# Kernel tuning notes

Hardware: AMD Instinct MI355X
Metric: run time of the kernel (lower is better)

The kernel has to match this reference:

```python
import jax, jax.numpy as jnp
import numpy as np

# SFNO (modulus) with spectral_transform='fft', filter_type='non-linear', scale_factor=1,
# hard_thresholding_fraction=1.0 (no mode truncation), instance_norm, inner_skip='linear',
# outer_skip='identity', use_mlp=True, encoder_layers=1, pos_embed, big_skip.
B, CIN, COUT, H, W = 1, 2, 2, 181, 360
E, HID, L = 128, 256, 4   # embed_dim, int(mlp_ratio*embed_dim), num_layers
EPS = 1e-6


def _inorm(x, w, b):
    # InstanceNorm2d(affine=True, eps=1e-6): per-(batch,channel) stats over H,W
    mu = jnp.mean(x, axis=(-2, -1), keepdims=True)
    var = jnp.var(x, axis=(-2, -1), keepdims=True)
    xh = (x - mu) * jax.lax.rsqrt(var + EPS)
    return xh * w[None, :, None, None] + b[None, :, None, None]


def _conv1x1(x, w, b=None):
    y = jnp.einsum('bihw,oi->bohw', x, w)
    return y if b is None else y + b[None, :, None, None]


def _cmul(z, w):
    # complex channel mixing; w stored as [2(re/im), c_in, c_out] float
    return jnp.einsum('bihw,io->bohw', z, w[0] + 1j * w[1])


def _crelu(z):
    # ComplexReLU mode='real': relu on real part, imaginary part passes through
    return jax.lax.complex(jax.nn.relu(z.real), z.imag)


def _block(x, p):
    (n0w, n0b, w0, w1, wout, isw, isb, n1w, n1b, fc1w, fc1b, fc2w, fc2b) = p
    xn = _inorm(x, n0w, n0b)
    # SpectralAttention2d (bias=False): rfft2 -> complex MLP over channels -> irfft2
    z = jnp.fft.rfft2(xn, axes=(-2, -1), norm='ortho')   # [B,E,H,W//2+1] complex
    h = _crelu(_cmul(z, w0))
    h = _crelu(_cmul(h, w1))
    y = jnp.fft.irfft2(_cmul(h, wout), s=(H, W), axes=(-2, -1), norm='ortho')
    y = y + _conv1x1(xn, isw, isb)                        # inner skip (linear 1x1 conv)
    y = _inorm(y, n1w, n1b)
    y = _conv1x1(jax.nn.gelu(_conv1x1(y, fc1w, fc1b), approximate=False), fc2w, fc2b)  # MLP
    return y + xn                                         # outer skip (identity on filter residual)


def _forward(x, enc_w0, enc_b0, enc_w1, pos_embed, n0w, n0b, w0, w1, wout,
             isw, isb, n1w, n1b, fc1w, fc1b, fc2w, fc2b, dec_w0, dec_b0, dec_w1):
    resid = x                                              # big skip
    h = jax.nn.gelu(_conv1x1(x, enc_w0, enc_b0), approximate=False)
    h = _conv1x1(h, enc_w1) + pos_embed                    # encoder (final conv bias=False) + pos embed
    def body(c, p):
        return _block(c, p), None
    h, _ = jax.lax.scan(body, h, (n0w, n0b, w0, w1, wout, isw, isb, n1w, n1b,
                                  fc1w, fc1b, fc2w, fc2b))
    h = jnp.concatenate([h, resid], axis=1)                # big skip concat
    h = jax.nn.gelu(_conv1x1(h, dec_w0, dec_b0), approximate=False)
    return _conv1x1(h, dec_w1)                             # decoder final conv bias=False


def setup_inputs() -> dict:
    key = jax.random.key(0)
    ks = jax.random.split(key, 16)
    s = 0.02  # scale used for spectral weights in SpectralAttention2d
    rn = lambda k, shp, sc: (sc * jax.random.normal(k, shp)).astype(jnp.float32)
    return {
        'x': rn(ks[0], (B, CIN, H, W), 1.0),
        'enc_w0': rn(ks[1], (E, CIN), 0.1),
        'enc_b0': jnp.zeros((E,), jnp.float32),
        'enc_w1': rn(ks[2], (E, E), 0.05),
        'pos_embed': rn(ks[3], (1, E, H, W), s),
        'n0w': jnp.ones((L, E), jnp.float32), 'n0b': jnp.zeros((L, E), jnp.float32),
        'w0': rn(ks[4], (L, 2, E, HID), s),
        'w1': rn(ks[5], (L, 2, HID, HID), s),
        'wout': rn(ks[6], (L, 2, HID, E), s),
        'isw': rn(ks[7], (L, E, E), 0.05), 'isb': jnp.zeros((L, E), jnp.float32),
        'n1w': jnp.ones((L, E), jnp.float32), 'n1b': jnp.zeros((L, E), jnp.float32),
        'fc1w': rn(ks[8], (L, HID, E), 0.05), 'fc1b': jnp.zeros((L, HID), jnp.float32),
        'fc2w': rn(ks[9], (L, E, HID), 0.05), 'fc2b': jnp.zeros((L, E), jnp.float32),
        'dec_w0': rn(ks[10], (E, E + CIN), 0.05),
        'dec_b0': jnp.zeros((E,), jnp.float32),
        'dec_w1': rn(ks[11], (COUT, E), 0.05),
    }


def reference(x, enc_w0, enc_b0, enc_w1, pos_embed, n0w, n0b, w0, w1, wout,
              isw, isb, n1w, n1b, fc1w, fc1b, fc2w, fc2b, dec_w0, dec_b0, dec_w1):
    return _forward(x, enc_w0, enc_b0, enc_w1, pos_embed, n0w, n0b, w0, w1, wout,
                    isw, isb, n1w, n1b, fc1w, fc1b, fc2w, fc2b, dec_w0, dec_b0, dec_w1)
```

## Files before the change

kernel.cpp:

```cpp
#include <hip/hip_runtime.h>
#include <math.h>

#define NP 65160
#define NPAD 65280

typedef unsigned short u16;
typedef __attribute__((ext_vector_type(8))) short bf16x8;
typedef __attribute__((ext_vector_type(8))) unsigned short us8;
typedef __attribute__((ext_vector_type(4))) float f32x4;

__device__ __forceinline__ u16 f2bf(float f){
    unsigned u = __builtin_bit_cast(unsigned, f);
    return (u16)((u + 0x7FFFu + ((u>>16)&1u)) >> 16);
}
__device__ __forceinline__ float bf2f(u16 h){
    unsigned u = ((unsigned)h)<<16;
    return __builtin_bit_cast(float, u);
}
__device__ __forceinline__ float gelu_f(float x){
    return 0.5f*x*(1.0f+erff(x*0.70710678118654752f));
}

__global__ void k_zero(u16* __restrict__ p, long n){
    long i = ((long)blockIdx.x*256 + threadIdx.x)*8;
    if(i+8 <= n){ us8 z = {0,0,0,0,0,0,0,0}; *(us8*)(p+i) = z; }
}

__global__ void k_pack_twf(u16* __restrict__ dst){
    int i = blockIdx.x*256+threadIdx.x; if(i >= 48*384*8) return;
    int e = i&7, n = (i>>3)%384, kg = i/(384*8);
    int k = kg*8+e, kw = n>>1, q = n&1;
    float v = 0.0f;
    if(k < 360 && kw < 181){
        float inv = 1.0f/sqrtf(65160.0f);
        float th = 6.28318530717958647692f*(float)((k*kw)%360)/360.0f;
        v = q ? -sinf(th)*inv : cosf(th)*inv;
    }
    dst[i] = f2bf(v);
}
__global__ void k_pack_thf(u16* __restrict__ dst){
    int i = blockIdx.x*256+threadIdx.x; if(i >= 64*384*8) return;
    int e = i&7, n = (i>>3)%384, kg = i/(384*8);
    int k = kg*8+e;
    float v = 0.0f;
    if(k < 362 && n < 362){
        int h = k>>1, q = k&1, kh = n>>1, p = n&1;
        float th = 6.28318530717958647692f*(float)((h*kh)%181)/181.0f;
        float c = cosf(th), s = sinf(th);
        v = (q==0) ? (p==0? c : -s) : (p==0? s : c);
    }
    dst[i] = f2bf(v);
}
__global__ void k_pack_thi(u16* __restrict__ dst){
    int i = blockIdx.x*256+threadIdx.x; if(i >= 48*384*8) return;
    int e = i&7, n = (i>>3)%384, kg = i/(384*8);
    int k = kg*8+e;
    float v = 0.0f;
    if(k < 362 && n < 362){
        int kh = k>>1, p = k&1, h = n>>1, q = n&1;
        float th = 6.28318530717958647692f*(float)((kh*h)%181)/181.0f;
        float c = cosf(th), s = sinf(th);
        v = (q==0) ? (p==0? c : -s) : (p==0? s : c);
    }
    dst[i] = f2bf(v);
}
__global__ void k_pack_twi(u16* __restrict__ dst){
    int i = blockIdx.x*256+threadIdx.x; if(i >= 48*384*8) return;
    int e = i&7, n = (i>>3)%384, kg = i/(384*8);
    int k = kg*8+e, kw = k>>1, q = k&1;
    float v = 0.0f;
    if(k < 362 && n < 360){
        float inv = 1.0f/sqrtf(65160.0f);
        float eps = (kw==0 || kw==180) ? 1.0f : 2.0f;
        float th = 6.28318530717958647692f*(float)((n*kw)%360)/360.0f;
        v = q ? -eps*sinf(th)*inv : eps*cosf(th)*inv;
    }
    dst[i] = f2bf(v);
}
__global__ void k_pack_cw(const float* __restrict__ src, u16* __restrict__ dst,
                          int CIN, int COUT, int lss, int lsd){
    int z = blockIdx.z;
    int Npad = 2*COUT, KG = (2*CIN)/8;
    int tot = KG*Npad*8;
    int i = blockIdx.x*256+threadIdx.x; if(i >= tot) return;
    int e = i&7, n = (i>>3)%Npad, kg = i/(Npad*8);
    int k = kg*8+e, ci = k>>1, q = k&1, co = n>>1, p = n&1;
    float re = src[(size_t)z*lss + ci*COUT + co];
    float im = src[(size_t)z*lss + CIN*COUT + ci*COUT + co];
    float v = (p==0) ? (q==0? re : -im) : (q==0? im : re);
    dst[(size_t)z*lsd + i] = f2bf(v);
}
__global__ void k_pack_rw(const float* __restrict__ src, u16* __restrict__ dst,
                          int Nn, int Ks, int KG, int lss, int lsd){
    int z = blockIdx.z;
    int tot = KG*Nn*8;
    int i = blockIdx.x*256+threadIdx.x; if(i >= tot) return;
    int e = i&7, n = (i>>3)%Nn, kg = i/(Nn*8);
    int k = kg*8+e;
    float v = (k < Ks) ? src[(size_t)z*lss + n*Ks + k] : 0.0f;
    dst[(size_t)z*lsd + i] = f2bf(v);
}

__global__ void k_enc0(const float* __restrict__ x, const float* __restrict__ w,
                       const float* __restrict__ b, u16* __restrict__ out){
    int i = blockIdx.x*256+threadIdx.x;
    if(i >= NP*16) return;
    int p = i>>4, c8 = (i&15)*8;
    float x0 = x[p], x1 = x[NP+p];
    us8 o;
    #pragma unroll
    for(int j=0;j<8;j++){
        int e = c8+j;
        float v = w[e*2]*x0 + w[e*2+1]*x1 + b[e];
        o[j] = f2bf(gelu_f(v));
    }
    *(us8*)(out + (size_t)p*128 + c8) = o;
}
__global__ void k_xt2(const float* __restrict__ x, u16* __restrict__ dst){
    int p = blockIdx.x*256+threadIdx.x; if(p >= NP) return;
    us8 z = {0,0,0,0,0,0,0,0};
    z[0] = f2bf(x[p]); z[1] = f2bf(x[NP+p]);
    *(us8*)(dst + (size_t)p*32) = z;
    us8 z2 = {0,0,0,0,0,0,0,0};
    *(us8*)(dst + (size_t)p*32 + 8)  = z2;
    *(us8*)(dst + (size_t)p*32 + 16) = z2;
    *(us8*)(dst + (size_t)p*32 + 24) = z2;
}
__global__ void k_dec1(const u16* __restrict__ hid, const float* __restrict__ w,
                       float* __restrict__ out){
    int p = blockIdx.x*256+threadIdx.x; if(p >= NP) return;
    float a0=0.0f, a1=0.0f;
    #pragma unroll 4
    for(int k8=0;k8<16;k8++){
        us8 v = *(const us8*)(hid + (size_t)p*128 + k8*8);
        #pragma unroll
        for(int j=0;j<8;j++){
            float f = bf2f(v[j]);
            a0 = fmaf(w[k8*8+j], f, a0);
            a1 = fmaf(w[128+k8*8+j], f, a1);
        }
    }
    out[p] = a0; out[NP+p] = a1;
}

__global__ __launch_bounds__(256) void k_apply_t(
    const u16* __restrict__ X, u16* __restrict__ outp, u16* __restrict__ outc,
    const float* __restrict__ stat, const float* __restrict__ gw, const float* __restrict__ gb)
{
    __shared__ u16 T[128][72];
    __shared__ float SA_[128], SB_[128];
    int t = threadIdx.x;
    if(t < 128){
        float mu = stat[t]*(1.0f/(float)NP);
        float var = stat[128+t]*(1.0f/(float)NP) - mu*mu;
        var = fmaxf(var, 0.0f);
        float rstd = 1.0f/sqrtf(var + 1e-6f);
        float a = rstd*gw[t];
        SA_[t] = a; SB_[t] = gb[t] - mu*a;
    }
    __syncthreads();
    int p0 = blockIdx.x*64;
    int pl = t>>2, cc = (t&3)*32;
    int p = p0 + pl;
    if(p < NP){
        #pragma unroll
        for(int jj=0;jj<4;jj++){
            us8 v = *(const us8*)(X + (size_t)p*128 + cc + jj*8);
            us8 o;
            #pragma unroll
            for(int j=0;j<8;j++){
                int c = cc + jj*8 + j;
                o[j] = f2bf(fmaf(bf2f(v[j]), SA_[c], SB_[c]));
            }
            *(us8*)(outp + (size_t)p*128 + cc + jj*8) = o;
            #pragma unroll
            for(int j=0;j<8;j++) T[cc+jj*8+j][pl] = o[j];
        }
    }
    __syncthreads();
    int c = t>>1, half = t&1;
    int pbase = p0 + half*32;
    #pragma unroll
    for(int jj=0;jj<4;jj++){
        int pp = pbase + jj*8;
        if(pp + 8 <= NP){
            int hh = pp/360, ww = pp - hh*360;
            *(us8*)(outc + ((size_t)c*192 + hh)*384 + ww) = *(const us8*)(&T[c][half*32 + jj*8]);
        }
    }
}
__global__ __launch_bounds__(256) void k_post(const float* __restrict__ src, u16* __restrict__ dst){
    __shared__ u16 T[128][72];
    int t = threadIdx.x;
    int p0 = blockIdx.x*64;
    int c = t>>1, half = t&1;
    int pbase = p0 + half*32;
    #pragma unroll
    for(int jj=0;jj<4;jj++){
        int pp = pbase + jj*8;
        us8 v = {0,0,0,0,0,0,0,0};
        if(pp + 8 <= NP){
            #pragma unroll
            for(int j=0;j<8;j++) v[j] = f2bf(src[(size_t)c*NP + pp + j]);
        }
        *(us8*)(&T[c][half*32 + jj*8]) = v;
    }
    __syncthreads();
    int pl = t>>2, cc = (t&3)*32;
    int p = p0 + pl;
    if(p < NP){
        #pragma unroll
        for(int jj=0;jj<4;jj++){
            us8 o;
            #pragma unroll
            for(int j=0;j<8;j++) o[j] = T[cc+jj*8+j][pl];
            *(us8*)(dst + (size_t)p*128 + cc + jj*8) = o;
        }
    }
}

__global__ __launch_bounds__(512, 4) void k_smlp(
    const u16* __restrict__ A3, const u16* __restrict__ W0,
    const u16* __restrict__ W1, const u16* __restrict__ WO,
    u16* __restrict__ A4)
{
    __shared__ u16 Hs0[32*520];
    __shared__ u16 Hs1[32*520];
    int tid = threadIdx.x;
    int l = tid & 63, wn = tid >> 6;
    int lm = l & 15, kg = l >> 4;
    int m0 = blockIdx.x * 32;

    f32x4 acc[2][4];
    #pragma unroll
    for(int f=0;f<2;f++)
        #pragma unroll
        for(int j2=0;j2<4;j2++) acc[f][j2] = (f32x4){0.f,0.f,0.f,0.f};
    {
        const u16* ap = A3 + (size_t)(m0 + lm)*256 + kg*8;
        #pragma unroll
        for(int k0=0;k0<256;k0+=32){
            bf16x8 af[2];
            #pragma unroll
            for(int f=0;f<2;f++) af[f] = *(const bf16x8*)(ap + f*16*256 + k0);
            const u16* Bb = W0 + (size_t)((k0>>3)+kg)*4096 + (wn*64+lm)*8;
            #pragma unroll
            for(int j2=0;j2<4;j2++){
                bf16x8 bf = *(const bf16x8*)(Bb + j2*128);
                #pragma unroll
                for(int f=0;f<2;f++)
                    acc[f][j2] = __builtin_amdgcn_mfma_f32_16x16x32_bf16(af[f], bf, acc[f][j2], 0,0,0);
            }
        }
    }
    #pragma unroll
    for(int f=0;f<2;f++)
        #pragma unroll
        for(int j2=0;j2<4;j2++)
            #pragma unroll
            for(int r=0;r<4;r++){
                int row = f*16 + kg*4 + r;
                int col = wn*64 + j2*16 + lm;
                float v = acc[f][j2][r];
                if(!(col&1)) v = fmaxf(v, 0.0f);
                Hs0[row*520 + col] = f2bf(v);
            }
    __syncthreads();
    #pragma unroll
    for(int f=0;f<2;f++)
        #pragma unroll
        for(int j2=0;j2<4;j2++) acc[f][j2] = (f32x4){0.f,0.f,0.f,0.f};
    #pragma unroll 2
    for(int k0=0;k0<512;k0+=32){
        bf16x8 af[2];
        #pragma unroll
        for(int f=0;f<2;f++) af[f] = *(const bf16x8*)(&Hs0[(f*16+lm)*520 + k0 + kg*8]);
        const u16* Bb = W1 + (size_t)((k0>>3)+kg)*4096 + (wn*64+lm)*8;
        #pragma unroll
        for(int j2=0;j2<4;j2++){
            bf16x8 bf = *(const bf16x8*)(Bb + j2*128);
            #pragma unroll
            for(int f=0;f<2;f++)
                acc[f][j2] = __builtin_amdgcn_mfma_f32_16x16x32_bf16(af[f], bf, acc[f][j2], 0,0,0);
        }
    }
    #pragma unroll
    for(int f=0;f<2;f++)
        #pragma unroll
        for(int j2=0;j2<4;j2++)
            #pragma unroll
            for(int r=0;r<4;r++){
                int row = f*16 + kg*4 + r;
                int col = wn*64 + j2*16 + lm;
                float v = acc[f][j2][r];
                if(!(col&1)) v = fmaxf(v, 0.0f);
                Hs1[row*520 + col] = f2bf(v);
            }
    __syncthreads();
    f32x4 acc3[2][2];
    #pragma unroll
    for(int f=0;f<2;f++)
        #pragma unroll
        for(int j2=0;j2<2;j2++) acc3[f][j2] = (f32x4){0.f,0.f,0.f,0.f};
    #pragma unroll 2
    for(int k0=0;k0<512;k0+=32){
        bf16x8 af[2];
        #pragma unroll
        for(int f=0;f<2;f++) af[f] = *(const bf16x8*)(&Hs1[(f*16+lm)*520 + k0 + kg*8]);
        const u16* Bb = WO + (size_t)((k0>>3)+kg)*2048 + (wn*32+lm)*8;
        #pragma unroll
        for(int j2=0;j2<2;j2++){
            bf16x8 bf = *(const bf16x8*)(Bb + j2*128);
            #pragma unroll
            for(int f=0;f<2;f++)
                acc3[f][j2] = __builtin_amdgcn_mfma_f32_16x16x32_bf16(af[f], bf, acc3[f][j2], 0,0,0);
        }
    }
    #pragma unroll
    for(int f=0;f<2;f++)
        #pragma unroll
        for(int j2=0;j2<2;j2++)
            #pragma unroll
            for(int r=0;r<4;r++){
                int row = f*16 + kg*4 + r;
                int col = wn*32 + j2*16 + lm;
                Hs0[row*258 + col] = f2bf(acc3[f][j2][r]);
            }
    __syncthreads();
    int kw = m0 / 192;
    int kh0 = m0 - kw*192;
    int c = tid >> 2, q = tid & 3;
    long base = ((long)(c*192 + kw))*384 + 2*(kh0 + q*8);
    #pragma unroll
    for(int jj=0;jj<2;jj++){
        us8 v;
        #pragma unroll
        for(int i=0;i<4;i++){
            v[2*i]   = Hs0[(q*8 + jj*4 + i)*258 + 2*c];
            v[2*i+1] = Hs0[(q*8 + jj*4 + i)*258 + 2*c+1];
        }
        *(us8*)(A4 + base + jj*8) = v;
    }
}

__global__ __launch_bounds__(512) void k_pmlp(
    const u16* __restrict__ A, const u16* __restrict__ FC1, const u16* __restrict__ FC2,
    const float* __restrict__ b1, const float* __restrict__ b2,
    const float* __restrict__ stat, const float* __restrict__ gw, const float* __restrict__ gb,
    const u16* __restrict__ addb, u16* __restrict__ OUT, float* __restrict__ statout)
{
    __shared__ u16 Hs[64][264];
    __shared__ float SA_[128], SB_[128];
    __shared__ float SS[128], SS2[128];
    int tid = threadIdx.x;
    int l = tid & 63, wv = tid >> 6;
    int wm = wv >> 1, wn = wv & 1;
    int lm = l & 15, kg = l >> 4;
    int m0 = blockIdx.x * 64;
    if(tid < 128){
        float mu = stat[tid]*(1.0f/(float)NP);
        float var = stat[128+tid]*(1.0f/(float)NP) - mu*mu;
        var = fmaxf(var, 0.0f);
        float rstd = 1.0f/sqrtf(var + 1e-6f);
        float a = rstd*gw[tid];
        SA_[tid] = a; SB_[tid] = gb[tid] - mu*a;
        SS[tid] = 0.0f; SS2[tid] = 0.0f;
    }
    __syncthreads();

    f32x4 acc[8];
    #pragma unroll
    for(int j=0;j<8;j++) acc[j] = (f32x4){0.f,0.f,0.f,0.f};
    {
        const u16* ap = A + (size_t)(m0 + wm*16 + lm)*128 + kg*8;
        #pragma unroll
        for(int k0=0;k0<128;k0+=32){
            us8 raw = *(const us8*)(ap + k0);
            bf16x8 af;
            #pragma unroll
            for(int j=0;j<8;j++){
                int ch = kg*8 + k0 + j;
                af[j] = (short)f2bf(fmaf(bf2f(raw[j]), SA_[ch], SB_[ch]));
            }
            const u16* Bb = FC1 + (size_t)((k0>>3)+kg)*2048 + (wn*128+lm)*8;
            #pragma unroll
            for(int j2=0;j2<8;j2++){
                bf16x8 bf = *(const bf16x8*)(Bb + j2*128);
                acc[j2] = __builtin_amdgcn_mfma_f32_16x16x32_bf16(af, bf, acc[j2], 0,0,0);
            }
        }
    }
    #pragma unroll
    for(int j2=0;j2<8;j2++)
        #pragma unroll
        for(int r=0;r<4;r++){
            int row = wm*16 + kg*4 + r;
            int col = wn*128 + j2*16 + lm;
            Hs[row][col] = f2bf(gelu_f(acc[j2][r] + b1[col]));
        }
    __syncthreads();
    f32x4 acc2[4];
    #pragma unroll
    for(int j=0;j<4;j++) acc2[j] = (f32x4){0.f,0.f,0.f,0.f};
    #pragma unroll
    for(int k0=0;k0<256;k0+=32){
        bf16x8 af = *(const bf16x8*)(&Hs[wm*16 + lm][k0 + kg*8]);
        const u16* Bb = FC2 + (size_t)((k0>>3)+kg)*1024 + (wn*64+lm)*8;
        #pragma unroll
        for(int j2=0;j2<4;j2++){
            bf16x8 bf = *(const bf16x8*)(Bb + j2*128);
            acc2[j2] = __builtin_amdgcn_mfma_f32_16x16x32_bf16(af, bf, acc2[j2], 0,0,0);
        }
    }
    float ts[4] = {0.f,0.f,0.f,0.f}, ts2[4] = {0.f,0.f,0.f,0.f};
    #pragma unroll
    for(int j2=0;j2<4;j2++)
        #pragma unroll
        for(int r=0;r<4;r++){
            int row = wm*16 + kg*4 + r;
            long p = m0 + row;
            if(p < NP){
                int n = wn*64 + j2*16 + lm;
                float v = acc2[j2][r] + b2[n] + bf2f(addb[p*128 + n]);
                u16 hv = f2bf(v);
                OUT[p*128 + n] = hv;
                float vq = bf2f(hv);
                ts[j2] += vq; ts2[j2] = fmaf(vq, vq, ts2[j2]);
            }
        }
    #pragma unroll
    for(int j2=0;j2<4;j2++){
        int n = wn*64 + j2*16 + lm;
        atomicAdd(&SS[n], ts[j2]);
        atomicAdd(&SS2[n], ts2[j2]);
    }
    __syncthreads();
    if(tid < 128){
        atomicAdd(&statout[tid], SS[tid]);
        atomicAdd(&statout[128+tid], SS2[tid]);
    }
}

template<int TMODE>
__global__ __launch_bounds__(512, 4) void k_gemmw(
    const u16* __restrict__ A, const u16* __restrict__ B, u16* __restrict__ C)
{
    __shared__ u16 Ts[64*392];
    int tid = threadIdx.x;
    int l = tid & 63, wv = tid >> 6;
    int lm = l & 15, kg = l >> 4;
    int m0 = blockIdx.x * 64;

    const u16* ap = A + (size_t)(m0 + lm)*384 + kg*8;
    int bn[3];
    #pragma unroll
    for(int j2=0;j2<3;j2++) bn[j2] = (wv*48 + j2*16 + lm)*8 + kg*3072;

    f32x4 acc[4][3];
    #pragma unroll
    for(int f=0;f<4;f++)
        #pragma unroll
        for(int j2=0;j2<3;j2++) acc[f][j2] = (f32x4){0.f,0.f,0.f,0.f};

    #pragma unroll
    for(int ks=0; ks<12; ks++){
        const int k0 = ks*32;
        bf16x8 af[4];
        #pragma unroll
        for(int f=0;f<4;f++) af[f] = *(const bf16x8*)(ap + f*16*384 + k0);
        const u16* Bb = B + (size_t)(ks*4)*3072;
        bf16x8 bf[3];
        #pragma unroll
        for(int j2=0;j2<3;j2++) bf[j2] = *(const bf16x8*)(Bb + bn[j2]);
        #pragma unroll
        for(int f=0;f<4;f++)
            #pragma unroll
            for(int j2=0;j2<3;j2++)
                acc[f][j2] = __builtin_amdgcn_mfma_f32_16x16x32_bf16(af[f], bf[j2], acc[f][j2], 0,0,0);
    }

    #pragma unroll
    for(int f=0;f<4;f++)
        #pragma unroll
        for(int j2=0;j2<3;j2++)
            #pragma unroll
            for(int r=0;r<4;r++)
                Ts[(f*16 + kg*4 + r)*392 + wv*48 + j2*16 + lm] = f2bf(acc[f][j2][r]);
    __syncthreads();

    if constexpr (TMODE != 5){
        #pragma unroll
        for(int it=0; it<6; it++){
            int g = tid + it*512;
            int gn = g % 192, gm = g / 192;
            int ml = gm*4, nl = gn*2;
            int mg = m0 + ml, ng = nl;
            long base;
            if constexpr (TMODE == 1){
                int c = (int)(((unsigned)mg*43691u)>>23);
                int sub = mg - c*192;
                base = ((long)((ng>>1)*128 + c))*384 + 2*sub;
            } else {
                int kw = mg>>7, c = mg&127;
                base = ((long)(kw*192 + (ng>>1)))*256 + 2*c;
            }
            us8 v;
            #pragma unroll
            for(int i=0;i<4;i++){
                v[2*i]   = Ts[(ml+i)*392 + nl];
                v[2*i+1] = Ts[(ml+i)*392 + nl+1];
            }
            *(us8*)(C + base) = v;
        }
    } else {
        #pragma unroll
        for(int it=0; it<6; it++){
            int g = tid + it*512;
            int nl = g % 384, gm = g / 384;
            int ml = gm*8;
            int mg = m0 + ml;
            if(nl < 360){
                int h = mg >> 7;
                long base = ((long)(h*360 + nl))*128 + (mg & 127);
                us8 v;
                #pragma unroll
                for(int j=0;j<8;j++) v[j] = Ts[(ml+j)*392 + nl];
                *(us8*)(C + base) = v;
            }
        }
    }
}

template<int KSTEPS, bool SPLIT, bool STATS>
__global__ __launch_bounds__(256, 2) void k_gemm(
    const u16* __restrict__ A1, const u16* __restrict__ A2, int aksplit, int astr, int a2str,
    const u16* __restrict__ B, int bkstr,
    u16* __restrict__ C, int cstr,
    const float* __restrict__ bias, const u16* __restrict__ addb,
    float* __restrict__ statout,
    int Mvalid, int N, int flags)
{
    __shared__ float SS[128], SS2[128];
    int tid = threadIdx.x;
    int l = tid & 63, wv = tid >> 6;
    int wm = wv >> 1, wn = wv & 1;
    int lm = l & 15, kgl = l >> 4;
    int m0 = blockIdx.y*128 + wm*64;
    int n0 = blockIdx.x*128 + wn*64;

    if constexpr (STATS){
        if(tid < 128){ SS[tid] = 0.0f; SS2[tid] = 0.0f; }
        __syncthreads();
    }

    int ab1[4], ab2[4];
    #pragma unroll
    for(int i2=0;i2<4;i2++){
        int mi = m0 + i2*16 + lm;
        ab1[i2] = mi*astr + kgl*8;
        ab2[i2] = mi*a2str + kgl*8;
    }
    int bn[4];
    #pragma unroll
    for(int j2=0;j2<4;j2++) bn[j2] = (n0 + j2*16 + lm)*8 + kgl*bkstr;

    f32x4 acc[4][4];
    #pragma unroll
    for(int i2=0;i2<4;i2++)
        #pragma unroll
        for(int j2=0;j2<4;j2++)
            acc[i2][j2] = (f32x4){0.0f,0.0f,0.0f,0.0f};

    #pragma unroll
    for(int ks=0; ks<KSTEPS; ks++){
        const int k0 = ks*32;
        bf16x8 af[4];
        if constexpr (SPLIT){
            int kk = k0 + kgl*8;
            bool s1v = kk < aksplit;
            #pragma unroll
            for(int i2=0;i2<4;i2++)
                af[i2] = s1v ? *(const bf16x8*)(A1 + ab1[i2] + k0)
                             : *(const bf16x8*)(A2 + ab2[i2] + k0 - aksplit);
        } else {
            #pragma unroll
            for(int i2=0;i2<4;i2++)
                af[i2] = *(const bf16x8*)(A1 + ab1[i2] + k0);
        }
        const u16* Bb = B + (size_t)(ks*4)*bkstr;
        bf16x8 bf[4];
        #pragma unroll
        for(int j2=0;j2<4;j2++)
            bf[j2] = *(const bf16x8*)(Bb + bn[j2]);
        #pragma unroll
        for(int i2=0;i2<4;i2++)
            #pragma unroll
            for(int j2=0;j2<4;j2++)
                acc[i2][j2] = __builtin_amdgcn_mfma_f32_16x16x32_bf16(af[i2], bf[j2], acc[i2][j2], 0,0,0);
    }

    float ts[4] = {0.f,0.f,0.f,0.f}, ts2[4] = {0.f,0.f,0.f,0.f};
    #pragma unroll
    for(int i2=0;i2<4;i2++){
        #pragma unroll
        for(int r=0;r<4;r++){
            int m = m0 + i2*16 + kgl*4 + r;
            if(m >= Mvalid) continue;
            long mb = (long)m*cstr;
            #pragma unroll
            for(int j2=0;j2<4;j2++){
                int n = n0 + j2*16 + lm;
                if(n >= N) continue;
                float v = acc[i2][j2][r];
                if(bias) v += bias[n];
                if(flags & 1) v = gelu_f(v);
                long ca = mb + n;
                if(addb) v += bf2f(addb[ca]);
                u16 hv = f2bf(v);
                C[ca] = hv;
                if constexpr (STATS){
                    float vq = bf2f(hv);
                    ts[j2] += vq; ts2[j2] = fmaf(vq, vq, ts2[j2]);
                }
            }
        }
    }
    if constexpr (STATS){
        #pragma unroll
        for(int j2=0;j2<4;j2++){
            int n = n0 + j2*16 + lm;
            atomicAdd(&SS[n], ts[j2]);
            atomicAdd(&SS2[n], ts2[j2]);
        }
        __syncthreads();
        if(tid < 128){
            atomicAdd(&statout[tid], SS[tid]);
            atomicAdd(&statout[128+tid], SS2[tid]);
        }
    }
}

extern "C" void kernel_launch(void* const* d_in, const int* in_sizes, int n_in,
                              void* d_out, int out_size, void* d_ws, size_t ws_size,
                              hipStream_t stream) {
    const float* x       = (const float*)d_in[0];
    const float* enc_w0  = (const float*)d_in[1];
    const float* enc_b0  = (const float*)d_in[2];
    const float* enc_w1  = (const float*)d_in[3];
    const float* pos     = (const float*)d_in[4];
    const float* n0w     = (const float*)d_in[5];
    const float* n0b     = (const float*)d_in[6];
    const float* w0      = (const float*)d_in[7];
    const float* w1      = (const float*)d_in[8];
    const float* wout    = (const float*)d_in[9];
    const float* isw     = (const float*)d_in[10];
    const float* isb     = (const float*)d_in[11];
    const float* n1w     = (const float*)d_in[12];
    const float* n1b     = (const float*)d_in[13];
    const float* fc1w    = (const float*)d_in[14];
    const float* fc1b    = (const float*)d_in[15];
    const float* fc2w    = (const float*)d_in[16];
    const float* fc2b    = (const float*)d_in[17];
    const float* dec_w0  = (const float*)d_in[18];
    const float* dec_b0  = (const float*)d_in[19];
    const float* dec_w1  = (const float*)d_in[20];
    float* out = (float*)d_out;

    u16* ws = (u16*)d_ws;
    size_t off = 0;
    auto al = [&](size_t n){ u16* p = ws + off; off += (n + 63) & ~(size_t)63; return p; };
    u16* TWF  = al(147456);
    u16* THF  = al(196608);
    u16* THI  = al(147456);
    u16* TWI  = al(147456);
    u16* W0P  = al(524288);
    u16* W1P  = al(1048576);
    u16* WOP  = al(524288);
    u16* ISWP = al(65536);
    u16* FC1P = al(131072);
    u16* FC2P = al(131072);
    u16* EW1P = al(16384);
    u16* DW0P = al(20480);
    u16* POSP = al((size_t)NPAD*128);
    u16* XT2  = al((size_t)NPAD*32);
    u16* CURP = al((size_t)NPAD*128);
    u16* XNP  = al((size_t)NPAD*128);
    u16* YP   = al((size_t)NPAD*128);
    u16* XNC  = al((size_t)24576*384);
    u16* A2b  = al((size_t)24576*384);
    u16* A3b  = al((size_t)36864*256);
    u16* A4b  = al((size_t)24576*384);
    u16* BIG  = al((size_t)NPAD*128);
    u16* IST  = al(5120);
    float* ISTAT = (float*)IST;
    u16* A5b = A2b;
    u16* ENC = BIG;

    dim3 blk(256);
    k_zero<<<dim3(4608), blk, 0, stream>>>(XNC, (long)24576*384);
    k_zero<<<dim3(3),    blk, 0, stream>>>(IST, 5120);

    k_pack_twf<<<dim3((147456+255)/256), blk, 0, stream>>>(TWF);
    k_pack_thf<<<dim3((196608+255)/256), blk, 0, stream>>>(THF);
    k_pack_thi<<<dim3((147456+255)/256), blk, 0, stream>>>(THI);
    k_pack_twi<<<dim3((147456+255)/256), blk, 0, stream>>>(TWI);
    k_pack_cw<<<dim3((131072+255)/256,1,4), blk, 0, stream>>>(w0,   W0P, 128, 256, 2*128*256, 131072);
    k_pack_cw<<<dim3((262144+255)/256,1,4), blk, 0, stream>>>(w1,   W1P, 256, 256, 2*256*256, 262144);
    k_pack_cw<<<dim3((131072+255)/256,1,4), blk, 0, stream>>>(wout, WOP, 256, 128, 2*256*128, 131072);
    k_pack_rw<<<dim3((16384+255)/256,1,4),  blk, 0, stream>>>(isw,  ISWP, 128, 128, 16, 128*128, 16384);
    k_pack_rw<<<dim3((32768+255)/256,1,4),  blk, 0, stream>>>(fc1w, FC1P, 256, 128, 16, 256*128, 32768);
    k_pack_rw<<<dim3((32768+255)/256,1,4),  blk, 0, stream>>>(fc2w, FC2P, 128, 256, 32, 128*256, 32768);
    k_pack_rw<<<dim3((16384+255)/256,1,1),  blk, 0, stream>>>(enc_w1, EW1P, 128, 128, 16, 0, 0);
    k_pack_rw<<<dim3((20480+255)/256,1,1),  blk, 0, stream>>>(dec_w0, DW0P, 128, 130, 20, 0, 0);
    k_post<<<dim3(1019), blk, 0, stream>>>(pos, POSP);
    k_xt2 <<<dim3((NP+255)/256), blk, 0, stream>>>(x, XT2);

    const u16* nu = nullptr;
    const float* nf = nullptr;
    const int BIGV = 1<<28;

    k_enc0<<<dim3((NP*16+255)/256), blk, 0, stream>>>(x, enc_w0, enc_b0, ENC);
    k_gemm<4,false,true><<<dim3(1,510), blk, 0, stream>>>(
        ENC, ENC, BIGV, 128, 128, EW1P, 1024, CURP, 128, nf, POSP,
        ISTAT + 0, NP, 128, 0);

    for(int l=0; l<4; l++){
        float* st0 = ISTAT + (2*l)*256;
        float* st1 = ISTAT + (2*l+1)*256;
        float* st0n = ISTAT + (2*l+2)*256;
        k_apply_t<<<dim3(1019), blk, 0, stream>>>(CURP, XNP, XNC, st0, n0w+l*128, n0b+l*128);
        k_gemmw<1><<<dim3(384), dim3(512), 0, stream>>>(XNC, TWF, A2b);
        k_gemmw<2><<<dim3(384), dim3(512), 0, stream>>>(A2b, THF, A3b);
        k_smlp<<<dim3(1152), dim3(512), 0, stream>>>(A3b,
            W0P + (size_t)l*131072, W1P + (size_t)l*262144, WOP + (size_t)l*131072, A4b);
        k_gemmw<1><<<dim3(384), dim3(512), 0, stream>>>(A4b, THI, A5b);
        k_gemmw<5><<<dim3(362), dim3(512), 0, stream>>>(A5b, TWI, YP);
        k_gemm<4,false,true><<<dim3(1,510), blk, 0, stream>>>(
            XNP, XNP, BIGV, 128, 128, ISWP + (size_t)l*16384, 1024, CURP, 128,
            isb+l*128, YP, st1, NP, 128, 0);
        k_pmlp<<<dim3(1019), dim3(512), 0, stream>>>(CURP,
            FC1P + (size_t)l*32768, FC2P + (size_t)l*32768,
            fc1b + l*256, fc2b + l*128,
            st1, n1w + l*128, n1b + l*128, XNP, CURP, st0n);
    }
    k_gemm<5,true,false><<<dim3(1,510), blk, 0, stream>>>(
        CURP, XT2, 128, 128, 32, DW0P, 1024, XNP, 128, dec_b0, nu,
        (float*)nullptr, NP, 128, 1);
    k_dec1<<<dim3((NP+255)/256), blk, 0, stream>>>(XNP, dec_w1, out);
}
```

Before: 1.462 ms.

## Double k_pmlp rows per block and use tanh-approximate GELU

k_pmlp now processes 128 rows per block instead of 64. Each wave computes two 16-row fragments, so every FC1/FC2 weight fragment it loads feeds two MFMAs, and the grid is halved. Separately, the exact erf-based GELU is replaced with the tanh approximation built on __expf, to cut the cost of the transcendental. Both accumulator sets double in size and launch_bounds(512,4) is requested, which risks register spills. The GELU change also departs numerically from the exact GELU the reference specifies.

```diff
diff --git a/kernel.cpp b/kernel.cpp
--- a/kernel.cpp
+++ b/kernel.cpp
@@ -18,7 +18,10 @@
     return __builtin_bit_cast(float, u);
 }
 __device__ __forceinline__ float gelu_f(float x){
-    return 0.5f*x*(1.0f+erff(x*0.70710678118654752f));
+    float z = 0.7978845608028654f*(x + 0.044715f*x*x*x);
+    float e = __expf(2.0f*z);
+    float t = 1.0f - 2.0f/(e + 1.0f);
+    return 0.5f*x*(1.0f + t);
 }
 
 __global__ void k_zero(u16* __restrict__ p, long n){
@@ -343,20 +346,20 @@
     }
 }
 
-__global__ __launch_bounds__(512) void k_pmlp(
+__global__ __launch_bounds__(512, 4) void k_pmlp(
     const u16* __restrict__ A, const u16* __restrict__ FC1, const u16* __restrict__ FC2,
     const float* __restrict__ b1, const float* __restrict__ b2,
     const float* __restrict__ stat, const float* __restrict__ gw, const float* __restrict__ gb,
     const u16* __restrict__ addb, u16* __restrict__ OUT, float* __restrict__ statout)
 {
-    __shared__ u16 Hs[64][264];
+    __shared__ u16 Hs[128][264];
     __shared__ float SA_[128], SB_[128];
     __shared__ float SS[128], SS2[128];
     int tid = threadIdx.x;
     int l = tid & 63, wv = tid >> 6;
     int wm = wv >> 1, wn = wv & 1;
     int lm = l & 15, kg = l >> 4;
-    int m0 = blockIdx.x * 64;
+    int m0 = blockIdx.x * 128;
     if(tid < 128){
         float mu = stat[tid]*(1.0f/(float)NP);
         float var = stat[128+tid]*(1.0f/(float)NP) - mu*mu;
@@ -368,66 +371,84 @@
     }
     __syncthreads();
 
-    f32x4 acc[8];
-    #pragma unroll
-    for(int j=0;j<8;j++) acc[j] = (f32x4){0.f,0.f,0.f,0.f};
+    f32x4 acc[2][8];
+    #pragma unroll
+    for(int f=0;f<2;f++)
+        #pragma unroll
+        for(int j=0;j<8;j++) acc[f][j] = (f32x4){0.f,0.f,0.f,0.f};
     {
-        const u16* ap = A + (size_t)(m0 + wm*16 + lm)*128 + kg*8;
+        const u16* ap = A + (size_t)(m0 + wm*32 + lm)*128 + kg*8;
         #pragma unroll
         for(int k0=0;k0<128;k0+=32){
-            us8 raw = *(const us8*)(ap + k0);
-            bf16x8 af;
-            #pragma unroll
-            for(int j=0;j<8;j++){
-                int ch = kg*8 + k0 + j;
-                af[j] = (short)f2bf(fmaf(bf2f(raw[j]), SA_[ch], SB_[ch]));
+            bf16x8 af[2];
+            #pragma unroll
+            for(int f=0;f<2;f++){
+                us8 raw = *(const us8*)(ap + f*16*128 + k0);
+                #pragma unroll
+                for(int j=0;j<8;j++){
+                    int ch = kg*8 + k0 + j;
+                    af[f][j] = (short)f2bf(fmaf(bf2f(raw[j]), SA_[ch], SB_[ch]));
+                }
             }
             const u16* Bb = FC1 + (size_t)((k0>>3)+kg)*2048 + (wn*128+lm)*8;
             #pragma unroll
             for(int j2=0;j2<8;j2++){
                 bf16x8 bf = *(const bf16x8*)(Bb + j2*128);
-                acc[j2] = __builtin_amdgcn_mfma_f32_16x16x32_bf16(af, bf, acc[j2], 0,0,0);
-            }
-        }
-    }
-    #pragma unroll
-    for(int j2=0;j2<8;j2++)
-        #pragma unroll
-        for(int r=0;r<4;r++){
-            int row = wm*16 + kg*4 + r;
-            int col = wn*128 + j2*16 + lm;
-            Hs[row][col] = f2bf(gelu_f(acc[j2][r] + b1[col]));
-        }
-    __syncthreads();
-    f32x4 acc2[4];
-    #pragma unroll
-    for(int j=0;j<4;j++) acc2[j] = (f32x4){0.f,0.f,0.f,0.f};
+                #pragma unroll
+                for(int f=0;f<2;f++)
+                    acc[f][j2] = __builtin_amdgcn_mfma_f32_16x16x32_bf16(af[f], bf, acc[f][j2], 0,0,0);
+            }
+        }
+    }
+    #pragma unroll
+    for(int f=0;f<2;f++)
+        #pragma unroll
+        for(int j2=0;j2<8;j2++)
+            #pragma unroll
+            for(int r=0;r<4;r++){
+                int row = wm*32 + f*16 + kg*4 + r;
+                int col = wn*128 + j2*16 + lm;
+                Hs[row][col] = f2bf(gelu_f(acc[f][j2][r] + b1[col]));
+            }
+    __syncthreads();
+    f32x4 acc2[2][4];
+    #pragma unroll
+    for(int f=0;f<2;f++)
+        #pragma unroll
+        for(int j=0;j<4;j++) acc2[f][j] = (f32x4){0.f,0.f,0.f,0.f};
     #pragma unroll
     for(int k0=0;k0<256;k0+=32){
-        bf16x8 af = *(const bf16x8*)(&Hs[wm*16 + lm][k0 + kg*8]);
+        bf16x8 af[2];
+        #pragma unroll
+        for(int f=0;f<2;f++)
+            af[f] = *(const bf16x8*)(&Hs[wm*32 + f*16 + lm][k0 + kg*8]);
         const u16* Bb = FC2 + (size_t)((k0>>3)+kg)*1024 + (wn*64+lm)*8;
         #pragma unroll
         for(int j2=0;j2<4;j2++){
             bf16x8 bf = *(const bf16x8*)(Bb + j2*128);
-            acc2[j2] = __builtin_amdgcn_mfma_f32_16x16x32_bf16(af, bf, acc2[j2], 0,0,0);
+            #pragma unroll
+            for(int f=0;f<2;f++)
+                acc2[f][j2] = __builtin_amdgcn_mfma_f32_16x16x32_bf16(af[f], bf, acc2[f][j2], 0,0,0);
         }
     }
     float ts[4] = {0.f,0.f,0.f,0.f}, ts2[4] = {0.f,0.f,0.f,0.f};
     #pragma unroll
-    for(int j2=0;j2<4;j2++)
-        #pragma unroll
-        for(int r=0;r<4;r++){
-            int row = wm*16 + kg*4 + r;
-            long p = m0 + row;
-            if(p < NP){
-                int n = wn*64 + j2*16 + lm;
-                float v = acc2[j2][r] + b2[n] + bf2f(addb[p*128 + n]);
-                u16 hv = f2bf(v);
-                OUT[p*128 + n] = hv;
-                float vq = bf2f(hv);
-                ts[j2] += vq; ts2[j2] = fmaf(vq, vq, ts2[j2]);
-            }
-        }
+    for(int f=0;f<2;f++)
+        #pragma unroll
+        for(int j2=0;j2<4;j2++)
+            #pragma unroll
+            for(int r=0;r<4;r++){
+                int row = wm*32 + f*16 + kg*4 + r;
+                long p = m0 + row;
+                if(p < NP){
+                    int n = wn*64 + j2*16 + lm;
+                    float v = acc2[f][j2][r] + b2[n] + bf2f(addb[p*128 + n]);
+                    u16 hv = f2bf(v);
+                    OUT[p*128 + n] = hv;
+                    float vq = bf2f(hv);
+                    ts[j2] += vq; ts2[j2] = fmaf(vq, vq, ts2[j2]);
+                }
+            }
     #pragma unroll
     for(int j2=0;j2<4;j2++){
         int n = wn*64 + j2*16 + lm;
@@ -738,7 +759,7 @@
         k_gemm<4,false,true><<<dim3(1,510), blk, 0, stream>>>(
             XNP, XNP, BIGV, 128, 128, ISWP + (size_t)l*16384, 1024, CURP, 128,
             isb+l*128, YP, st1, NP, 128, 0);
-        k_pmlp<<<dim3(1019), dim3(512), 0, stream>>>(CURP,
+        k_pmlp<<<dim3(510), dim3(512), 0, stream>>>(CURP,
             FC1P + (size_t)l*32768, FC2P + (size_t)l*32768,
             fc1b + l*256, fc2b + l*128,
             st1, n1w + l*128, n1b + l*128, XNP, CURP, st0n);
```

After: 1.357 ms. 7.2% less time.
